# Performance work log

Measured on AMD Instinct MI355X. Metric: run time of the kernel, lower is better.

Reference implementation:

```python
import jax, jax.numpy as jnp
import numpy as np
import math

B, C, H, W = 8, 512, 32, 32
NUM_HEADS = 8          # channels // num_head_channels = 512 // 64
NUM_GROUPS = 32        # GroupNorm32
EPS = 1e-5


def setup_inputs() -> dict:
    key = jax.random.key(0)
    k1, k2, k3, k4, k5 = jax.random.split(key, 5)
    x = jax.random.normal(k1, (B, C, H, W), dtype=jnp.float32)
    # GroupNorm affine params (torch init: ones/zeros)
    norm_scale = jnp.ones((C,), dtype=jnp.float32)
    norm_bias = jnp.zeros((C,), dtype=jnp.float32)
    # 1x1 Conv1d weights: qkv maps C -> 3C, proj maps C -> C
    qkv_w = jax.random.normal(k2, (3 * C, C), dtype=jnp.float32) * 0.02
    qkv_b = jax.random.normal(k3, (3 * C,), dtype=jnp.float32) * 0.02
    # NOTE: original zero-inits proj_out; we use small random weights so the
    # block computes non-trivial math (same op structure, same FLOPs).
    proj_w = jax.random.normal(k4, (C, C), dtype=jnp.float32) * 0.02
    proj_b = jax.random.normal(k5, (C,), dtype=jnp.float32) * 0.02
    return {"x": x, "norm_scale": norm_scale, "norm_bias": norm_bias,
            "qkv_w": qkv_w, "qkv_b": qkv_b, "proj_w": proj_w, "proj_b": proj_b}


def _attention_block(x, norm_scale, norm_bias, qkv_w, qkv_b, proj_w, proj_b):
    b, c, h, w = x.shape
    t = h * w
    xf = x.reshape(b, c, t)
    # GroupNorm32: fp32 compute, 32 groups, biased variance, eps=1e-5
    g = xf.astype(jnp.float32).reshape(b, NUM_GROUPS, c // NUM_GROUPS, t)
    mean = g.mean(axis=(2, 3), keepdims=True)
    var = g.var(axis=(2, 3), keepdims=True)
    gn = ((g - mean) * jax.lax.rsqrt(var + EPS)).reshape(b, c, t)
    gn = (gn * norm_scale[None, :, None] + norm_bias[None, :, None]).astype(xf.dtype)
    # 1x1 conv == channel matmul: [B,C,T] -> [B,3C,T]
    qkv = jnp.einsum('oc,bct->bot', qkv_w, gn) + qkv_b[None, :, None]
    # Legacy head layout: [B, H*3*ch, T] -> [B*H, 3*ch, T]
    ch = c // NUM_HEADS
    qkv = qkv.reshape(b * NUM_HEADS, 3 * ch, t)
    q, k, v = jnp.split(qkv, 3, axis=1)          # each [B*H, ch, T]
    scale = 1.0 / math.sqrt(math.sqrt(ch))
    weight = jnp.einsum('bct,bcs->bts', q * scale, k * scale)  # [B*H, T, T]
    weight = jax.nn.softmax(weight.astype(jnp.float32), axis=-1).astype(qkv.dtype)
    a = jnp.einsum('bts,bcs->bct', weight, v).reshape(b, c, t)
    out = jnp.einsum('oc,bct->bot', proj_w, a) + proj_b[None, :, None]
    return (xf + out).reshape(b, c, h, w)


def reference(x, norm_scale, norm_bias, qkv_w, qkv_b, proj_w, proj_b):
    return _attention_block(x, norm_scale, norm_bias, qkv_w, qkv_b, proj_w, proj_b)
```

## Files before the change

### kernel.cpp

```cpp
#include <hip/hip_runtime.h>
#include <math.h>

#define B_   8
#define C_   512
#define T_   1024
#define G_   32
#define CPG  16
#define NH   8
#define OC3  1536
#define EPS  1e-5f

#define QSCALE 0.18033688011112042f
#define C_OFF  11.541560327111708f

typedef __bf16 bf16;
typedef __bf16 bf16x4 __attribute__((ext_vector_type(4)));
typedef __bf16 bf16x8 __attribute__((ext_vector_type(8)));
typedef float  f32x4  __attribute__((ext_vector_type(4)));
typedef short  s16x4  __attribute__((ext_vector_type(4)));

#define MFMA16(a, b, c) __builtin_amdgcn_mfma_f32_16x16x32_bf16((a), (b), (c), 0, 0, 0)

__device__ __forceinline__ f32x4 mfma_k16(bf16x4 a, bf16x4 b, f32x4 c) {
#if __has_builtin(__builtin_amdgcn_mfma_f32_16x16x16_bf16)
    return __builtin_amdgcn_mfma_f32_16x16x16_bf16(a, b, c, 0, 0, 0);
#else
    return __builtin_amdgcn_mfma_f32_16x16x16bf16_1k(
        __builtin_bit_cast(s16x4, a), __builtin_bit_cast(s16x4, b), c, 0, 0, 0);
#endif
}

__device__ __forceinline__ float fexp2(float x) {
#if defined(__has_builtin)
#if __has_builtin(__builtin_amdgcn_exp2f)
    return __builtin_amdgcn_exp2f(x);
#else
    return __expf(x * 0.6931471805599453f);
#endif
#else
    return __expf(x * 0.6931471805599453f);
#endif
}

__global__ __launch_bounds__(256) void pre_kernel(const float* __restrict__ w1,
                                                  bf16* __restrict__ wb1,
                                                  const float* __restrict__ w2,
                                                  bf16* __restrict__ wb2,
                                                  const float* __restrict__ x,
                                                  const float* __restrict__ scale,
                                                  const float* __restrict__ bias,
                                                  bf16* __restrict__ gnT)
{
    const int blk0 = blockIdx.x;
    const int tid = threadIdx.x;
    if (blk0 < 1024) {
        const float* src = (blk0 < 768) ? w1 : w2;
        bf16* dst        = (blk0 < 768) ? wb1 : wb2;
        int i = (blk0 < 768 ? blk0 : blk0 - 768) * 256 + tid;
        float4 v = ((const float4*)src)[i];
        bf16x4 o;
        o[0] = (bf16)v.x; o[1] = (bf16)v.y; o[2] = (bf16)v.z; o[3] = (bf16)v.w;
        *(bf16x4*)(dst + (size_t)i * 4) = o;
        return;
    }
    const int blk = blk0 - 1024;
    const int b = blk >> 5, g = blk & 31;
    const size_t base = (size_t)blk * (CPG * T_);
    const float4* xin = (const float4*)(x + base);

    float s = 0.f, ss = 0.f;
    float4 vals[16];
#pragma unroll
    for (int i = 0; i < 16; ++i) {
        float4 v = xin[tid + i * 256];
        vals[i] = v;
        s  += v.x + v.y + v.z + v.w;
        ss += v.x * v.x + v.y * v.y + v.z * v.z + v.w * v.w;
    }

    __shared__ float rs[256], rss[256];
    rs[tid] = s; rss[tid] = ss;
    __syncthreads();
    for (int off = 128; off > 0; off >>= 1) {
        if (tid < off) { rs[tid] += rs[tid + off]; rss[tid] += rss[tid + off]; }
        __syncthreads();
    }
    const float invN = 1.f / (float)(CPG * T_);
    const float mean = rs[0] * invN;
    const float var  = rss[0] * invN - mean * mean;
    const float inv  = rsqrtf(var + EPS);

    const int c0 = g * CPG;
    float sc[16], bi[16];
#pragma unroll
    for (int i = 0; i < 16; ++i) {
        float s_ = scale[c0 + i] * inv;
        sc[i] = s_;
        bi[i] = bias[c0 + i] - mean * s_;
    }
    bf16* ob = gnT + (size_t)b * (T_ * C_) + c0;
#pragma unroll
    for (int tt = 0; tt < 4; ++tt) {
        bf16x8 lo, hi;
#pragma unroll
        for (int i = 0; i < 8; ++i) {
            float v0 = (tt == 0) ? vals[i].x : (tt == 1) ? vals[i].y
                     : (tt == 2) ? vals[i].z : vals[i].w;
            float v1 = (tt == 0) ? vals[i + 8].x : (tt == 1) ? vals[i + 8].y
                     : (tt == 2) ? vals[i + 8].z : vals[i + 8].w;
            lo[i] = (bf16)(v0 * sc[i] + bi[i]);
            hi[i] = (bf16)(v1 * sc[i + 8] + bi[i + 8]);
        }
        bf16* p = ob + (size_t)(4 * tid + tt) * C_;
        *(bf16x8*)p       = lo;
        *(bf16x8*)(p + 8) = hi;
    }
}

template <int MODE>
__global__ __launch_bounds__(256) void mm128(const bf16* __restrict__ Arows,
                                             const bf16* __restrict__ Wt,
                                             const float* __restrict__ bias,
                                             const float* __restrict__ x,
                                             void* __restrict__ outp)
{
    const int b   = blockIdx.z;
    const int o0  = blockIdx.y * 128;
    const int t0  = blockIdx.x * 128;
    const int tid = threadIdx.x;
    const int lane = tid & 63;
    const int w  = tid >> 6;
    const int wr = w >> 1, wc = w & 1;
    const int lq = lane & 15, lg = lane >> 4;

    __shared__ __align__(16) bf16 Ag[128][72];
    __shared__ __align__(16) bf16 Bg[128][72];

    const bf16* gA = Arows + (size_t)b * (T_ * C_) + (size_t)t0 * C_;
    const bf16* gB = Wt + (size_t)o0 * C_;

    f32x4 acc[4][4];
#pragma unroll
    for (int i = 0; i < 4; ++i)
#pragma unroll
        for (int j = 0; j < 4; ++j) { acc[i][j][0]=0.f; acc[i][j][1]=0.f; acc[i][j][2]=0.f; acc[i][j][3]=0.f; }

    bf16x8 areg[4], breg[4];
#pragma unroll
    for (int it = 0; it < 4; ++it) {
        int chunk = it * 256 + tid, row = chunk >> 3, cp = chunk & 7;
        areg[it] = *(const bf16x8*)(gA + (size_t)row * C_ + cp * 8);
        breg[it] = *(const bf16x8*)(gB + (size_t)row * C_ + cp * 8);
    }

    for (int k0 = 0; k0 < C_; k0 += 64) {
        __syncthreads();
#pragma unroll
        for (int it = 0; it < 4; ++it) {
            int chunk = it * 256 + tid, row = chunk >> 3, cp = chunk & 7;
            *(bf16x8*)&Ag[row][cp * 8] = areg[it];
            *(bf16x8*)&Bg[row][cp * 8] = breg[it];
        }
        __syncthreads();
        if (k0 + 64 < C_) {
#pragma unroll
            for (int it = 0; it < 4; ++it) {
                int chunk = it * 256 + tid, row = chunk >> 3, cp = chunk & 7;
                areg[it] = *(const bf16x8*)(gA + (size_t)row * C_ + k0 + 64 + cp * 8);
                breg[it] = *(const bf16x8*)(gB + (size_t)row * C_ + k0 + 64 + cp * 8);
            }
        }
#pragma unroll
        for (int kb = 0; kb < 2; ++kb) {
            bf16x8 af[4], bfr[4];
#pragma unroll
            for (int i = 0; i < 4; ++i) {
                af[i]  = *(const bf16x8*)&Ag[wr * 64 + i * 16 + lq][kb * 32 + lg * 8];
                bfr[i] = *(const bf16x8*)&Bg[wc * 64 + i * 16 + lq][kb * 32 + lg * 8];
            }
#pragma unroll
            for (int mf = 0; mf < 4; ++mf)
#pragma unroll
                for (int nf = 0; nf < 4; ++nf)
                    acc[mf][nf] = MFMA16(af[mf], bfr[nf], acc[mf][nf]);
        }
    }

    if (MODE == 0) {
        bf16* qkvT = (bf16*)outp;
#pragma unroll
        for (int nf = 0; nf < 4; ++nf) {
            int chg = o0 + wc * 64 + nf * 16 + lq;
            int seg = chg >> 6;
            int which = seg % 3;
            int chs = chg & 63;
            float bv = bias[chg];
            bf16* outb = qkvT + (size_t)(b * 24 + seg) * (T_ * 64);
            if (which != 2) {
                float osc = (which == 0) ? QSCALE : 1.0f;
#pragma unroll
                for (int mf = 0; mf < 4; ++mf) {
                    int tb = t0 + wr * 64 + mf * 16 + lg * 4;
#pragma unroll
                    for (int r = 0; r < 4; ++r)
                        outb[(size_t)(tb + r) * 64 + chs] = (bf16)((acc[mf][nf][r] + bv) * osc);
                }
            } else {
#pragma unroll
                for (int mf = 0; mf < 4; ++mf) {
                    int tb = t0 + wr * 64 + mf * 16 + lg * 4;
                    bf16x4 pb;
#pragma unroll
                    for (int r = 0; r < 4; ++r) pb[r] = (bf16)(acc[mf][nf][r] + bv);
                    *(bf16x4*)(outb + (size_t)chs * T_ + tb) = pb;
                }
            }
        }
    } else {
        float* out = (float*)outp;
#pragma unroll
        for (int nf = 0; nf < 4; ++nf) {
            int o = o0 + wc * 64 + nf * 16 + lq;
            float bv = bias[o];
#pragma unroll
            for (int mf = 0; mf < 4; ++mf) {
                int tb = t0 + wr * 64 + mf * 16 + lg * 4;
                size_t idx = ((size_t)b * C_ + o) * T_ + tb;
                float4 xr = *(const float4*)(x + idx);
                float4 rv;
                rv.x = acc[mf][nf][0] + bv + xr.x;
                rv.y = acc[mf][nf][1] + bv + xr.y;
                rv.z = acc[mf][nf][2] + bv + xr.z;
                rv.w = acc[mf][nf][3] + bv + xr.w;
                *(float4*)(out + idx) = rv;
            }
        }
    }
}

__global__ __launch_bounds__(512) void attn_kernel(const bf16* __restrict__ qkvT,
                                                   bf16* __restrict__ aT)
{
    const int id = blockIdx.x;
    const int bh = id & 63;
    const int tile = id >> 6;
    const int tid = threadIdx.x;
    const int lane = tid & 63;
    const int w  = tid >> 6;
    const int lq = lane & 15;
    const int lg = lane >> 4;
    const int q0 = tile * 128 + w * 16;

    const bf16* qb = qkvT + (size_t)(bh * 3 + 0) * (T_ * 64);
    const bf16* kb = qkvT + (size_t)(bh * 3 + 1) * (T_ * 64);
    const bf16* vb = qkvT + (size_t)(bh * 3 + 2) * (T_ * 64);

    __shared__ __align__(16) bf16 ks[64][72];
    __shared__ __align__(16) bf16 vs[64][136];

    bf16x8 qf[2];
#pragma unroll
    for (int kh = 0; kh < 2; ++kh)
        qf[kh] = *(const bf16x8*)(qb + (size_t)(q0 + lq) * 64 + kh * 32 + lg * 8);

    f32x4 oacc[4], lacc;
    lacc[0]=0.f; lacc[1]=0.f; lacc[2]=0.f; lacc[3]=0.f;
#pragma unroll
    for (int og = 0; og < 4; ++og) { oacc[og][0]=0.f; oacc[og][1]=0.f; oacc[og][2]=0.f; oacc[og][3]=0.f; }

    bf16x4 vones;
    vones[0] = (bf16)1.0f; vones[1] = (bf16)1.0f; vones[2] = (bf16)1.0f; vones[3] = (bf16)1.0f;

    const int sr = tid >> 3, scp = tid & 7;
    bf16x8 kreg, vreg;
    kreg = *(const bf16x8*)(kb + (size_t)sr * 64 + scp * 8);
    vreg = *(const bf16x8*)(vb + (size_t)sr * T_ + scp * 8);

    for (int i = 0; i < 16; ++i) {
        __syncthreads();
        *(bf16x8*)&ks[sr][scp * 8] = kreg;
        *(bf16x8*)&vs[sr][scp * 8] = vreg;
        __syncthreads();
        if (i < 15) {
            int sn = (i + 1) * 64;
            kreg = *(const bf16x8*)(kb + (size_t)(sn + sr) * 64 + scp * 8);
            vreg = *(const bf16x8*)(vb + (size_t)sr * T_ + sn + scp * 8);
        }

        f32x4 st[4];
        f32x4 cinit; cinit[0] = -C_OFF; cinit[1] = -C_OFF; cinit[2] = -C_OFF; cinit[3] = -C_OFF;
#pragma unroll
        for (int g = 0; g < 4; ++g) {
            bf16x8 kf0 = *(const bf16x8*)&ks[g * 16 + lq][lg * 8];
            bf16x8 kf1 = *(const bf16x8*)&ks[g * 16 + lq][32 + lg * 8];
            st[g] = MFMA16(kf0, qf[0], cinit);
            st[g] = MFMA16(kf1, qf[1], st[g]);
        }
        bf16x4 pa16[4];
#pragma unroll
        for (int g = 0; g < 4; ++g)
#pragma unroll
            for (int r = 0; r < 4; ++r)
                pa16[g][r] = (bf16)fexp2(st[g][r]);
#pragma unroll
        for (int g = 0; g < 4; ++g)
            lacc = mfma_k16(pa16[g], vones, lacc);
#pragma unroll
        for (int og = 0; og < 4; ++og) {
#pragma unroll
            for (int g = 0; g < 4; ++g) {
                bf16x4 vf = *(const bf16x4*)&vs[og * 16 + lq][g * 16 + lg * 4];
                oacc[og] = mfma_k16(pa16[g], vf, oacc[og]);
            }
        }
    }

    const int b = bh >> 3, h = bh & 7;
    float li[4];
#pragma unroll
    for (int r = 0; r < 4; ++r) li[r] = 1.f / lacc[r];
    bf16* ob = aT + ((size_t)b * T_ + q0 + lg * 4) * C_ + h * 64 + lq;
#pragma unroll
    for (int og = 0; og < 4; ++og)
#pragma unroll
        for (int r = 0; r < 4; ++r)
            ob[(size_t)r * C_ + og * 16] = (bf16)(oacc[og][r] * li[r]);
}

extern "C" void kernel_launch(void* const* d_in, const int* in_sizes, int n_in,
                              void* d_out, int out_size, void* d_ws, size_t ws_size,
                              hipStream_t stream)
{
    (void)in_sizes; (void)n_in; (void)out_size; (void)ws_size;
    const float* x      = (const float*)d_in[0];
    const float* nscale = (const float*)d_in[1];
    const float* nbias  = (const float*)d_in[2];
    const float* qkv_w  = (const float*)d_in[3];
    const float* qkv_b  = (const float*)d_in[4];
    const float* proj_w = (const float*)d_in[5];
    const float* proj_b = (const float*)d_in[6];
    float* out = (float*)d_out;

    char* wsb = (char*)d_ws;
    bf16*  gnT  = (bf16*) (wsb);
    bf16*  Wb   = (bf16*) (wsb + (size_t)(8  << 20));
    bf16*  PWb  = Wb + (size_t)OC3 * C_;
    bf16*  qkvT = (bf16*) (wsb + (size_t)(12 << 20));
    bf16*  aT   = (bf16*) (wsb + (size_t)(36 << 20));

    pre_kernel<<<1280, 256, 0, stream>>>(qkv_w, Wb, proj_w, PWb,
                                         x, nscale, nbias, gnT);
    mm128<0><<<dim3(T_ / 128, OC3 / 128, B_), 256, 0, stream>>>(gnT, Wb, qkv_b, nullptr, qkvT);
    attn_kernel<<<512, 512, 0, stream>>>(qkvT, aT);
    mm128<1><<<dim3(T_ / 128, C_ / 128, B_), 256, 0, stream>>>(aT, PWb, proj_b, x, out);
}
```

Before: 79.00 us.

## Use direct global-to-LDS loads in GEMM and enlarge attention KV tile

```diff
diff --git a/kernel.cpp b/kernel.cpp
--- a/kernel.cpp
+++ b/kernel.cpp
@@ -40,6 +40,12 @@
 #else
     return __expf(x * 0.6931471805599453f);
 #endif
+}
+
+typedef const __attribute__((address_space(1))) unsigned int* as1_u32p;
+typedef __attribute__((address_space(3))) unsigned int* as3_u32p;
+__device__ __forceinline__ void gload16(const bf16* g, bf16* lds_base) {
+    __builtin_amdgcn_global_load_lds((as1_u32p)g, (as3_u32p)lds_base, 16, 0, 0);
 }
 
 __global__ __launch_bounds__(256) void pre_kernel(const float* __restrict__ w1,
@@ -132,9 +138,10 @@
     const int w  = tid >> 6;
     const int wr = w >> 1, wc = w & 1;
     const int lq = lane & 15, lg = lane >> 4;
-
-    __shared__ __align__(16) bf16 Ag[128][72];
-    __shared__ __align__(16) bf16 Bg[128][72];
+    const int lrow = lane >> 3, lcol = lane & 7;
+
+    __shared__ __align__(16) bf16 Ag[128][64];
+    __shared__ __align__(16) bf16 Bg[128][64];
 
     const bf16* gA = Arows + (size_t)b * (T_ * C_) + (size_t)t0 * C_;
     const bf16* gB = Wt + (size_t)o0 * C_;
@@ -145,31 +152,14 @@
 #pragma unroll
         for (int j = 0; j < 4; ++j) { acc[i][j][0]=0.f; acc[i][j][1]=0.f; acc[i][j][2]=0.f; acc[i][j][3]=0.f; }
 
-    bf16x8 areg[4], breg[4];
-#pragma unroll
-    for (int it = 0; it < 4; ++it) {
-        int chunk = it * 256 + tid, row = chunk >> 3, cp = chunk & 7;
-        areg[it] = *(const bf16x8*)(gA + (size_t)row * C_ + cp * 8);
-        breg[it] = *(const bf16x8*)(gB + (size_t)row * C_ + cp * 8);
-    }
-
     for (int k0 = 0; k0 < C_; k0 += 64) {
-        __syncthreads();
-#pragma unroll
-        for (int it = 0; it < 4; ++it) {
-            int chunk = it * 256 + tid, row = chunk >> 3, cp = chunk & 7;
-            *(bf16x8*)&Ag[row][cp * 8] = areg[it];
-            *(bf16x8*)&Bg[row][cp * 8] = breg[it];
-        }
-        __syncthreads();
-        if (k0 + 64 < C_) {
-#pragma unroll
-            for (int it = 0; it < 4; ++it) {
-                int chunk = it * 256 + tid, row = chunk >> 3, cp = chunk & 7;
-                areg[it] = *(const bf16x8*)(gA + (size_t)row * C_ + k0 + 64 + cp * 8);
-                breg[it] = *(const bf16x8*)(gB + (size_t)row * C_ + k0 + 64 + cp * 8);
-            }
-        }
+#pragma unroll
+        for (int j = 0; j < 4; ++j) {
+            int rbase = w * 32 + j * 8;
+            gload16(gA + (size_t)(rbase + lrow) * C_ + k0 + lcol * 8, &Ag[rbase][0]);
+            gload16(gB + (size_t)(rbase + lrow) * C_ + k0 + lcol * 8, &Bg[rbase][0]);
+        }
+        __syncthreads();
 #pragma unroll
         for (int kb = 0; kb < 2; ++kb) {
             bf16x8 af[4], bfr[4];
@@ -184,6 +174,7 @@
                 for (int nf = 0; nf < 4; ++nf)
                     acc[mf][nf] = MFMA16(af[mf], bfr[nf], acc[mf][nf]);
         }
+        __syncthreads();
     }
 
     if (MODE == 0) {
@@ -255,8 +246,8 @@
     const bf16* kb = qkvT + (size_t)(bh * 3 + 1) * (T_ * 64);
     const bf16* vb = qkvT + (size_t)(bh * 3 + 2) * (T_ * 64);
 
-    __shared__ __align__(16) bf16 ks[64][72];
-    __shared__ __align__(16) bf16 vs[64][136];
+    __shared__ __align__(16) bf16 ks[128][72];
+    __shared__ __align__(16) bf16 vs[64][264];
 
     bf16x8 qf[2];
 #pragma unroll
@@ -271,46 +262,60 @@
     bf16x4 vones;
     vones[0] = (bf16)1.0f; vones[1] = (bf16)1.0f; vones[2] = (bf16)1.0f; vones[3] = (bf16)1.0f;
 
-    const int sr = tid >> 3, scp = tid & 7;
-    bf16x8 kreg, vreg;
-    kreg = *(const bf16x8*)(kb + (size_t)sr * 64 + scp * 8);
-    vreg = *(const bf16x8*)(vb + (size_t)sr * T_ + scp * 8);
-
-    for (int i = 0; i < 16; ++i) {
-        __syncthreads();
-        *(bf16x8*)&ks[sr][scp * 8] = kreg;
-        *(bf16x8*)&vs[sr][scp * 8] = vreg;
-        __syncthreads();
-        if (i < 15) {
-            int sn = (i + 1) * 64;
-            kreg = *(const bf16x8*)(kb + (size_t)(sn + sr) * 64 + scp * 8);
-            vreg = *(const bf16x8*)(vb + (size_t)sr * T_ + sn + scp * 8);
-        }
-
-        f32x4 st[4];
-        f32x4 cinit; cinit[0] = -C_OFF; cinit[1] = -C_OFF; cinit[2] = -C_OFF; cinit[3] = -C_OFF;
-#pragma unroll
-        for (int g = 0; g < 4; ++g) {
-            bf16x8 kf0 = *(const bf16x8*)&ks[g * 16 + lq][lg * 8];
-            bf16x8 kf1 = *(const bf16x8*)&ks[g * 16 + lq][32 + lg * 8];
-            st[g] = MFMA16(kf0, qf[0], cinit);
-            st[g] = MFMA16(kf1, qf[1], st[g]);
-        }
-        bf16x4 pa16[4];
-#pragma unroll
-        for (int g = 0; g < 4; ++g)
-#pragma unroll
-            for (int r = 0; r < 4; ++r)
-                pa16[g][r] = (bf16)fexp2(st[g][r]);
-#pragma unroll
-        for (int g = 0; g < 4; ++g)
-            lacc = mfma_k16(pa16[g], vones, lacc);
-#pragma unroll
-        for (int og = 0; og < 4; ++og) {
+    bf16x8 kreg[2], vreg[2];
+#pragma unroll
+    for (int it = 0; it < 2; ++it) {
+        int ck = it * 512 + tid;
+        kreg[it] = *(const bf16x8*)(kb + (size_t)(ck >> 3) * 64 + (ck & 7) * 8);
+        vreg[it] = *(const bf16x8*)(vb + (size_t)(ck >> 4) * T_ + (ck & 15) * 8);
+    }
+
+    for (int i = 0; i < 8; ++i) {
+        __syncthreads();
+#pragma unroll
+        for (int it = 0; it < 2; ++it) {
+            int ck = it * 512 + tid;
+            *(bf16x8*)&ks[ck >> 3][(ck & 7) * 8] = kreg[it];
+            *(bf16x8*)&vs[ck >> 4][(ck & 15) * 8] = vreg[it];
+        }
+        __syncthreads();
+        if (i < 7) {
+            int sn = (i + 1) * 128;
+#pragma unroll
+            for (int it = 0; it < 2; ++it) {
+                int ck = it * 512 + tid;
+                kreg[it] = *(const bf16x8*)(kb + (size_t)(sn + (ck >> 3)) * 64 + (ck & 7) * 8);
+                vreg[it] = *(const bf16x8*)(vb + (size_t)(ck >> 4) * T_ + sn + (ck & 15) * 8);
+            }
+        }
+
+#pragma unroll
+        for (int h = 0; h < 2; ++h) {
+            f32x4 st[4];
+            f32x4 cinit; cinit[0] = -C_OFF; cinit[1] = -C_OFF; cinit[2] = -C_OFF; cinit[3] = -C_OFF;
 #pragma unroll
             for (int g = 0; g < 4; ++g) {
-                bf16x4 vf = *(const bf16x4*)&vs[og * 16 + lq][g * 16 + lg * 4];
-                oacc[og] = mfma_k16(pa16[g], vf, oacc[og]);
+                bf16x8 kf0 = *(const bf16x8*)&ks[h * 64 + g * 16 + lq][lg * 8];
+                bf16x8 kf1 = *(const bf16x8*)&ks[h * 64 + g * 16 + lq][32 + lg * 8];
+                st[g] = MFMA16(kf0, qf[0], cinit);
+                st[g] = MFMA16(kf1, qf[1], st[g]);
+            }
+            bf16x4 pa16[4];
+#pragma unroll
+            for (int g = 0; g < 4; ++g)
+#pragma unroll
+                for (int r = 0; r < 4; ++r)
+                    pa16[g][r] = (bf16)fexp2(st[g][r]);
+#pragma unroll
+            for (int g = 0; g < 4; ++g)
+                lacc = mfma_k16(pa16[g], vones, lacc);
+#pragma unroll
+            for (int og = 0; og < 4; ++og) {
+#pragma unroll
+                for (int g = 0; g < 4; ++g) {
+                    bf16x4 vf = *(const bf16x4*)&vs[og * 16 + lq][h * 64 + g * 16 + lg * 4];
+                    oacc[og] = mfma_k16(pa16[g], vf, oacc[og]);
+                }
             }
         }
     }
```

New measurement: 90.83 us. +15.0%, slower.
